# Performance work log

Hardware: AMD Instinct MI355X
Metric: run time of the kernel (lower is better)

## Reference

```python
import jax, jax.numpy as jnp
import numpy as np

K = 3  # kernel size per dim
PAD = K // 2
CHANS = [1, 40, 80, 160, 80, 40, 1]  # channel ladder of the 6 convNd layers


def conv4d(x, w, b):
    """4D convolution, stride 1, 'same' padding.
    x: [B, Cin, D1, D2, D3, D4]; w: [Cout, Cin, K, K, K, K]; b: [Cout].
    Implemented as K shifted 3D convs along D1 (D1 folded into batch), summed.
    """
    B, Cin, D1, D2, D3, D4 = x.shape
    Cout = w.shape[0]
    # pad only D1 here; the inner conv pads D2..D4
    xp = jnp.pad(x, ((0, 0), (0, 0), (PAD, PAD), (0, 0), (0, 0), (0, 0)))
    xp = jnp.transpose(xp, (0, 2, 1, 3, 4, 5))  # [B, D1+2p, Cin, D2, D3, D4]
    dn = jax.lax.conv_dimension_numbers(
        (B * D1, Cin, D2, D3, D4), (Cout, Cin, K, K, K),
        ('NCDHW', 'OIDHW', 'NCDHW'))
    acc = None
    for i in range(K):  # small fixed loop over kernel taps along D1
        xs = xp[:, i:i + D1].reshape(B * D1, Cin, D2, D3, D4)
        y = jax.lax.conv_general_dilated(
            xs, w[:, :, i], window_strides=(1, 1, 1),
            padding=[(PAD, PAD)] * 3, dimension_numbers=dn)
        acc = y if acc is None else acc + y
    out = acc.reshape(B, D1, Cout, D2, D3, D4)
    out = jnp.transpose(out, (0, 2, 1, 3, 4, 5))
    return out + b[None, :, None, None, None, None]


def setup_inputs() -> dict:
    key = jax.random.key(0)
    kx, key = jax.random.split(key)
    inp = {'x': jax.random.normal(kx, (2, 1, 16, 16, 16, 16), dtype=jnp.float32)}
    for l in range(6):
        kw, key = jax.random.split(key)
        cin, cout = CHANS[l], CHANS[l + 1]
        std = (2.0 / (cin * K ** 4)) ** 0.5  # Kaiming-style fan-in init
        inp[f'w{l + 1}'] = jax.random.normal(kw, (cout, cin, K, K, K, K), dtype=jnp.float32) * std
        inp[f'b{l + 1}'] = jnp.zeros((cout,), dtype=jnp.float32)
    return inp


def reference(x, w1, b1, w2, b2, w3, b3, w4, b4, w5, b5, w6, b6):
    h = jax.nn.relu(conv4d(x, w1, b1))
    h = jax.nn.relu(conv4d(h, w2, b2))
    h = jax.nn.relu(conv4d(h, w3, b3))
    h = jax.nn.relu(conv4d(h, w4, b4))
    h = jax.nn.relu(conv4d(h, w5, b5))
    h = conv4d(h, w6, b6)
    return jax.nn.relu(h)
```

## Files before the change

kernel.cpp:

```cpp
#include <hip/hip_runtime.h>

typedef __attribute__((ext_vector_type(8))) short short8;
typedef __attribute__((ext_vector_type(4))) float f32x4;

#define GLD16(gsrc, ldst) __builtin_amdgcn_global_load_lds( \
    (const __attribute__((address_space(1))) unsigned int*)(gsrc), \
    (__attribute__((address_space(3))) unsigned int*)(ldst), 16, 0, 0)

__device__ __forceinline__ ushort f2bf(float f){
    union { float f; unsigned u; } v; v.f = f;
    unsigned r = (v.u + 0x7fffu + ((v.u >> 16) & 1u)) >> 16;
    return (ushort)r;
}
__device__ __forceinline__ float bf2f(ushort u){
    union { unsigned u; float f; } v; v.u = ((unsigned)u) << 16;
    return v.f;
}

__global__ __launch_bounds__(256) void conv_l1(
    const float* __restrict__ x, const float* __restrict__ w,
    const float* __restrict__ bias, ushort* __restrict__ out)
{
    __shared__ float xs[2916];
    __shared__ float wsh[3240];
    const int tid = threadIdx.x;
    const int bx = blockIdx.x;
    const int d2 = bx & 15, d1 = (bx >> 4) & 15, b = bx >> 8;
    const float* xb = x + (size_t)b * 65536;

    for (int i = tid; i < 2916; i += 256){
        int i4 = i % 18; int r1 = i / 18; int i3 = r1 % 18;
        int r2 = r1 / 18; int a2 = r2 % 3; int a1 = r2 / 3;
        int e1 = d1 + a1 - 1, e2 = d2 + a2 - 1, e3 = i3 - 1, e4 = i4 - 1;
        float v = 0.f;
        if ((unsigned)e1 < 16u && (unsigned)e2 < 16u && (unsigned)e3 < 16u && (unsigned)e4 < 16u)
            v = xb[((e1 * 16 + e2) * 16 + e3) * 16 + e4];
        xs[i] = v;
    }
    for (int i = tid; i < 3240; i += 256) wsh[i] = w[i];
    __syncthreads();

    const int d3 = tid >> 4, d4 = tid & 15;
    float acc[40];
    #pragma unroll
    for (int c = 0; c < 40; ++c) acc[c] = 0.f;

    for (int t1 = 0; t1 < 3; ++t1)
    for (int t2 = 0; t2 < 3; ++t2)
    for (int t3 = 0; t3 < 3; ++t3)
    #pragma unroll
    for (int t4 = 0; t4 < 3; ++t4){
        float xv = xs[((t1 * 3 + t2) * 18 + d3 + t3) * 18 + d4 + t4];
        int tap = ((t1 * 3 + t2) * 3 + t3) * 3 + t4;
        #pragma unroll
        for (int c = 0; c < 40; ++c) acc[c] += wsh[c * 81 + tap] * xv;
    }

    ushort* ob = out + ((size_t)bx * 256 + tid) * 64;
    #pragma unroll
    for (int c = 0; c < 40; ++c){
        float v = acc[c] + bias[c]; v = v > 0.f ? v : 0.f;
        ob[c] = f2bf(v);
    }
    #pragma unroll
    for (int c = 40; c < 64; ++c) ob[c] = 0;
}

__global__ __launch_bounds__(256) void conv_l6(
    const ushort* __restrict__ in, const float* __restrict__ w,
    const float* __restrict__ bias, float* __restrict__ out)
{
    __shared__ float wsh[3240];
    const int tid = threadIdx.x;
    const int bx = blockIdx.x;
    const int d2 = bx & 15, d1 = (bx >> 4) & 15, b = bx >> 8;
    for (int i = tid; i < 3240; i += 256) wsh[i] = w[i];
    __syncthreads();

    const int d3 = tid >> 4, d4 = tid & 15;
    const ushort* inb = in + (size_t)b * 65536 * 48;
    float acc = 0.f;
    for (int t1 = 0; t1 < 3; ++t1){
        int e1 = d1 + t1 - 1; if ((unsigned)e1 >= 16u) continue;
        for (int t2 = 0; t2 < 3; ++t2){
            int e2 = d2 + t2 - 1; if ((unsigned)e2 >= 16u) continue;
            for (int t3 = 0; t3 < 3; ++t3){
                int e3 = d3 + t3 - 1; if ((unsigned)e3 >= 16u) continue;
                for (int t4 = 0; t4 < 3; ++t4){
                    int e4 = d4 + t4 - 1; if ((unsigned)e4 >= 16u) continue;
                    const ushort* p = inb + (size_t)(((e1 * 16 + e2) * 16 + e3) * 16 + e4) * 48;
                    int tap = ((t1 * 3 + t2) * 3 + t3) * 3 + t4;
                    #pragma unroll
                    for (int c8 = 0; c8 < 5; ++c8){
                        short8 v = *(const short8*)(p + c8 * 8);
                        #pragma unroll
                        for (int j = 0; j < 8; ++j)
                            acc += bf2f((ushort)v[j]) * wsh[(c8 * 8 + j) * 81 + tap];
                    }
                }
            }
        }
    }
    float v = acc + bias[0]; v = v > 0.f ? v : 0.f;
    out[(size_t)bx * 256 + tid] = v;
}

__global__ void repack_wq(const float* __restrict__ w, ushort* __restrict__ wq,
                          int cin_real, int cout_real, int kc, int cout_w, int nstrip)
{
    const int ncc = 27 * kc;
    const int total = nstrip * ncc * 8192;
    for (int o = blockIdx.x * blockDim.x + threadIdx.x; o < total; o += gridDim.x * blockDim.x){
        const int j = o & 7;
        const int u_phys = (o >> 3) & 1023;
        const int chunk = o >> 13;
        const int strip = chunk / ncc;
        const int cc = chunk - strip * ncc;
        const int gg = cc / (kc * 3);
        const int rem = cc - gg * (kc * 3);
        const int kh = rem / 3;
        const int t3 = rem - kh * 3;
        float v = 0.f;
        if (u_phys < 12 * cout_w){
            const int per = 4 * cout_w;
            const int gk = ((u_phys % per) / cout_w) & 3;
            const int u = u_phys ^ gk;
            const int t4 = u / per;
            const int rest = u - t4 * per;
            const int gk2 = rest / cout_w;
            const int col = rest - gk2 * cout_w;
            const int tap = gg * 9 + t3 * 3 + t4;
            const int ci = kh * 32 + gk2 * 8 + j;
            const int co = strip * cout_w + col;
            if (ci < cin_real && co < cout_real)
                v = w[((size_t)co * cin_real + ci) * 81 + tap];
        }
        wq[o] = f2bf(v);
    }
}

template<int CIN_S, int COUT_W, int OST, int CREAL, int PADC>
__global__ __launch_bounds__(256, 2) void conv16(
    const ushort* __restrict__ in, const ushort* __restrict__ wq,
    const float* __restrict__ bias, ushort* __restrict__ out)
{
    constexpr int KC  = CIN_S / 32;
    constexpr int NT  = COUT_W / 16;
    constexpr int NCC = 27 * KC;
    constexpr int AH  = 18 * 18 * 32;

    __shared__ __attribute__((aligned(16))) ushort As[2][AH];
    __shared__ __attribute__((aligned(16))) ushort Bs[2][8192];

    const int tid  = threadIdx.x;
    const int lane = tid & 63;
    const int wm   = tid >> 6;
    const int r    = lane & 15;
    const int g    = lane >> 4;

    const int p0 = blockIdx.x;
    const int strip = p0 >> 9;
    const int pp = p0 & 511;
    const int bx = (pp & 7) * 64 + (pp >> 3);
    const int d2 = bx & 15, d1 = (bx >> 4) & 15, b = bx >> 8;
    const int co_base = strip * COUT_W;

    const ushort* inb = in + (size_t)b * 65536 * CIN_S;
    const ushort* wqs = wq + ((size_t)strip * NCC << 13);

    unsigned long long gpack = 0ull; int ng = 0;
    #pragma unroll
    for (int gg = 0; gg < 9; ++gg){
        const int t1 = gg / 3, t2 = gg - (gg / 3) * 3;
        if ((unsigned)(d1 + t1 - 1) < 16u && (unsigned)(d2 + t2 - 1) < 16u){
            gpack |= ((unsigned long long)gg) << (ng * 4);
            ++ng;
        }
    }
    const int nchunk = ng * KC;
    const int nstep  = nchunk * 3;

    f32x4 acc[4][NT];
    #pragma unroll
    for (int mi = 0; mi < 4; ++mi)
        #pragma unroll
        for (int n = 0; n < NT; ++n)
            acc[mi][n] = (f32x4){0.f, 0.f, 0.f, 0.f};

    const int ubase = (tid >> 6) * 256;
    const int ul = tid & 63;

    auto issueB = [&](int sn, ushort* dst){
        const int cc = sn / 3, tt = sn - cc * 3;
        const int gi = cc / KC, kh = cc - gi * KC;
        const int gg = (int)((gpack >> (gi * 4)) & 15ull);
        const ushort* src = wqs + ((size_t)((gg * KC + kh) * 3 + tt) << 13);
        #pragma unroll
        for (int k = 0; k < 4; ++k){
            const int u0 = ubase + k * 64;
            GLD16(src + (size_t)(u0 + ul) * 8, dst + u0 * 8);
        }
    };
    auto issueA = [&](int cn, ushort* dst){
        const int gi = cn / KC, kh = cn - gi * KC;
        const int gg = (int)((gpack >> (gi * 4)) & 15ull);
        const int t1 = gg / 3, t2 = gg - t1 * 3;
        const ushort* src = inb + ((size_t)((d1 + t1 - 1) * 16 + (d2 + t2 - 1)) * 256) * CIN_S + kh * 32;
        const int e4s = ul >> 2;
        const int gcs = (ul & 3) ^ ((ul >> 3) & 3);
        #pragma unroll
        for (int k = 0; k < 4; ++k){
            const int row = wm * 4 + k;
            GLD16(src + (size_t)(row * 16 + e4s) * CIN_S + gcs * 8,
                  dst + ((row + 1) * 18 + 1) * 32);
        }
    };

    {
        const short8 z = {0, 0, 0, 0, 0, 0, 0, 0};
        short8* a0 = (short8*)As[0];
        short8* a1 = (short8*)As[1];
        for (int i = tid; i < AH / 8; i += 256){ a0[i] = z; a1[i] = z; }
    }
    asm volatile("s_waitcnt lgkmcnt(0)" ::: "memory");
    __builtin_amdgcn_s_barrier();
    issueA(0, As[0]);
    issueB(0, Bs[0]);
    asm volatile("s_waitcnt vmcnt(0)" ::: "memory");
    __builtin_amdgcn_s_barrier();
    __builtin_amdgcn_sched_barrier(0);

    int c = 0, t3 = 0;
    for (int s = 0; s < nstep; ++s){
        int nis = 0;
        if (s + 1 < nstep){ issueB(s + 1, Bs[(s + 1) & 1]); nis += 4; }
        if (t3 == 0 && c + 1 < nchunk){ issueA(c + 1, As[(c + 1) & 1]); nis += 4; }
        if (nis == 8)      asm volatile("s_waitcnt vmcnt(8)" ::: "memory");
        else if (nis == 4) asm volatile("s_waitcnt vmcnt(4)" ::: "memory");
        else               asm volatile("s_waitcnt vmcnt(0)" ::: "memory");
        __builtin_amdgcn_s_barrier();
        __builtin_amdgcn_sched_barrier(0);

        const ushort* Ab = As[c & 1];
        const ushort* Bb = Bs[s & 1];
        __builtin_amdgcn_s_setprio(1);
        #pragma unroll
        for (int t4 = 0; t4 < 3; ++t4){
            const int e4 = r + t4 - 1;
            const int gsw = (g ^ ((e4 >> 1) & 3)) * 8;
            const ushort* arow = Ab + ((wm * 4 + t3) * 18 + (e4 + 1)) * 32 + gsw;
            short8 bfr[NT];
            #pragma unroll
            for (int n = 0; n < NT; ++n)
                bfr[n] = *(const short8*)(Bb + ((((t4 * 4 + g) * COUT_W + n * 16 + r) * 8) ^ (g << 3)));
            #pragma unroll
            for (int mi = 0; mi < 4; ++mi){
                const short8 af = *(const short8*)(arow + mi * (18 * 32));
                #pragma unroll
                for (int n = 0; n < NT; ++n)
                    acc[mi][n] = __builtin_amdgcn_mfma_f32_16x16x32_bf16(af, bfr[n], acc[mi][n], 0, 0, 0);
            }
        }
        __builtin_amdgcn_s_setprio(0);

        __builtin_amdgcn_sched_barrier(0);
        __builtin_amdgcn_s_barrier();
        __builtin_amdgcn_sched_barrier(0);

        ++t3; if (t3 == 3){ t3 = 0; ++c; }
    }

    float bv[NT];
    #pragma unroll
    for (int n = 0; n < NT; ++n){
        const int co = co_base + n * 16 + r;
        bv[n] = (co < CREAL) ? bias[co] : 0.f;
    }
    ushort* ob = out + (size_t)bx * 256 * OST;
    #pragma unroll
    for (int mi = 0; mi < 4; ++mi){
        #pragma unroll
        for (int n = 0; n < NT; ++n){
            const int co = co_base + n * 16 + r;
            #pragma unroll
            for (int j = 0; j < 4; ++j){
                const int row = 64 * wm + 16 * mi + g * 4 + j;
                float v = acc[mi][n][j] + bv[n];
                v = v > 0.f ? v : 0.f;
                ob[(size_t)row * OST + co] = f2bf(v);
            }
        }
    }
    if (PADC > 0){
        const int row = 64 * wm + lane;
        const short8 z = {0, 0, 0, 0, 0, 0, 0, 0};
        #pragma unroll
        for (int pc = 0; pc < PADC; pc += 8)
            *(short8*)(ob + (size_t)row * OST + CREAL + pc) = z;
    }
}

extern "C" void kernel_launch(void* const* d_in, const int* in_sizes, int n_in,
                              void* d_out, int out_size, void* d_ws, size_t ws_size,
                              hipStream_t stream) {
    const float* x  = (const float*)d_in[0];
    const float* w1 = (const float*)d_in[1];  const float* b1 = (const float*)d_in[2];
    const float* w2 = (const float*)d_in[3];  const float* b2 = (const float*)d_in[4];
    const float* w3 = (const float*)d_in[5];  const float* b3 = (const float*)d_in[6];
    const float* w4 = (const float*)d_in[7];  const float* b4 = (const float*)d_in[8];
    const float* w5 = (const float*)d_in[9];  const float* b5 = (const float*)d_in[10];
    const float* w6 = (const float*)d_in[11]; const float* b6 = (const float*)d_in[12];

    ushort* bufA = (ushort*)d_ws;
    ushort* bufB = bufA + (size_t)131072 * 160;
    ushort* wq2  = bufB + (size_t)131072 * 96;
    ushort* wq3  = wq2 + (size_t)54  * 8192;
    ushort* wq4  = wq3 + (size_t)162 * 8192;
    ushort* wq5  = wq4 + (size_t)135 * 8192;

    repack_wq<<<512, 256, 0, stream>>>(w2, wq2,  40,  80, 2, 80, 1);
    repack_wq<<<512, 256, 0, stream>>>(w3, wq3,  80, 160, 3, 80, 2);
    repack_wq<<<512, 256, 0, stream>>>(w4, wq4, 160,  80, 5, 80, 1);
    repack_wq<<<512, 256, 0, stream>>>(w5, wq5,  80,  40, 3, 48, 1);

    conv_l1<<<512, 256, 0, stream>>>(x, w1, b1, bufA);
    conv16<  64,   80,  96,  80,  16><<< 512, 256, 0, stream>>>(bufA, wq2, b2, bufB);
    conv16<  96,   80, 160, 160,   0><<<1024, 256, 0, stream>>>(bufB, wq3, b3, bufA);
    conv16< 160,   80,  96,  80,  16><<< 512, 256, 0, stream>>>(bufA, wq4, b4, bufB);
    conv16<  96,   48,  48,  40,   0><<< 512, 256, 0, stream>>>(bufB, wq5, b5, bufA);
    conv_l6<<<512, 256, 0, stream>>>(bufA, w6, b6, (float*)d_out);
}
```

Baseline: 814.0 us.

## Read weights directly from global memory and stage activations through registers

Drops the LDS double buffer for weight tiles: MFMA B fragments are now loaded straight from global memory (L1/L2 cached), and the repack no longer applies an XOR swizzle. Activation tiles are prefetched two chunks ahead into registers and written to LDS with ordinary stores, replacing the direct global-to-LDS async loads. Per-step barriers fall to one per chunk, and occupancy is raised to 3 blocks per CU because LDS use drops. In exchange, weight reads now stall the MFMA loop on global latency instead of being hidden behind an async prefetch, and register pressure goes up.

```diff
diff --git a/kernel.cpp b/kernel.cpp
--- a/kernel.cpp
+++ b/kernel.cpp
@@ -2,10 +2,6 @@
 
 typedef __attribute__((ext_vector_type(8))) short short8;
 typedef __attribute__((ext_vector_type(4))) float f32x4;
-
-#define GLD16(gsrc, ldst) __builtin_amdgcn_global_load_lds( \
-    (const __attribute__((address_space(1))) unsigned int*)(gsrc), \
-    (__attribute__((address_space(3))) unsigned int*)(ldst), 16, 0, 0)
 
 __device__ __forceinline__ ushort f2bf(float f){
     union { float f; unsigned u; } v; v.f = f;
@@ -112,7 +108,7 @@
     const int total = nstrip * ncc * 8192;
     for (int o = blockIdx.x * blockDim.x + threadIdx.x; o < total; o += gridDim.x * blockDim.x){
         const int j = o & 7;
-        const int u_phys = (o >> 3) & 1023;
+        const int u = (o >> 3) & 1023;
         const int chunk = o >> 13;
         const int strip = chunk / ncc;
         const int cc = chunk - strip * ncc;
@@ -121,16 +117,14 @@
         const int kh = rem / 3;
         const int t3 = rem - kh * 3;
         float v = 0.f;
-        if (u_phys < 12 * cout_w){
+        if (u < 12 * cout_w){
             const int per = 4 * cout_w;
-            const int gk = ((u_phys % per) / cout_w) & 3;
-            const int u = u_phys ^ gk;
             const int t4 = u / per;
             const int rest = u - t4 * per;
-            const int gk2 = rest / cout_w;
-            const int col = rest - gk2 * cout_w;
+            const int gk = rest / cout_w;
+            const int col = rest - gk * cout_w;
             const int tap = gg * 9 + t3 * 3 + t4;
-            const int ci = kh * 32 + gk2 * 8 + j;
+            const int ci = kh * 32 + gk * 8 + j;
             const int co = strip * cout_w + col;
             if (ci < cin_real && co < cout_real)
                 v = w[((size_t)co * cin_real + ci) * 81 + tap];
@@ -140,7 +134,7 @@
 }
 
 template<int CIN_S, int COUT_W, int OST, int CREAL, int PADC>
-__global__ __launch_bounds__(256, 2) void conv16(
+__global__ __launch_bounds__(256, 3) void conv16(
     const ushort* __restrict__ in, const ushort* __restrict__ wq,
     const float* __restrict__ bias, ushort* __restrict__ out)
 {
@@ -150,7 +144,6 @@
     constexpr int AH  = 18 * 18 * 32;
 
     __shared__ __attribute__((aligned(16))) ushort As[2][AH];
-    __shared__ __attribute__((aligned(16))) ushort Bs[2][8192];
 
     const int tid  = threadIdx.x;
     const int lane = tid & 63;
@@ -178,7 +171,6 @@
         }
     }
     const int nchunk = ng * KC;
-    const int nstep  = nchunk * 3;
 
     f32x4 acc[4][NT];
     #pragma unroll
@@ -187,32 +179,27 @@
         for (int n = 0; n < NT; ++n)
             acc[mi][n] = (f32x4){0.f, 0.f, 0.f, 0.f};
 
-    const int ubase = (tid >> 6) * 256;
-    const int ul = tid & 63;
-
-    auto issueB = [&](int sn, ushort* dst){
-        const int cc = sn / 3, tt = sn - cc * 3;
-        const int gi = cc / KC, kh = cc - gi * KC;
-        const int gg = (int)((gpack >> (gi * 4)) & 15ull);
-        const ushort* src = wqs + ((size_t)((gg * KC + kh) * 3 + tt) << 13);
-        #pragma unroll
-        for (int k = 0; k < 4; ++k){
-            const int u0 = ubase + k * 64;
-            GLD16(src + (size_t)(u0 + ul) * 8, dst + u0 * 8);
-        }
-    };
-    auto issueA = [&](int cn, ushort* dst){
-        const int gi = cn / KC, kh = cn - gi * KC;
+    short8 areg[4];
+    const int e4s = lane >> 2;
+    const int jl  = lane & 3;
+    const int gcs = jl ^ ((lane >> 3) & 3);
+
+    auto loadAreg = [&](int c){
+        const int gi = c / KC, kh = c - gi * KC;
         const int gg = (int)((gpack >> (gi * 4)) & 15ull);
         const int t1 = gg / 3, t2 = gg - t1 * 3;
         const ushort* src = inb + ((size_t)((d1 + t1 - 1) * 16 + (d2 + t2 - 1)) * 256) * CIN_S + kh * 32;
-        const int e4s = ul >> 2;
-        const int gcs = (ul & 3) ^ ((ul >> 3) & 3);
         #pragma unroll
         for (int k = 0; k < 4; ++k){
             const int row = wm * 4 + k;
-            GLD16(src + (size_t)(row * 16 + e4s) * CIN_S + gcs * 8,
-                  dst + ((row + 1) * 18 + 1) * 32);
+            areg[k] = *(const short8*)(src + (size_t)(row * 16 + e4s) * CIN_S + gcs * 8);
+        }
+    };
+    auto writeA = [&](ushort* dst){
+        #pragma unroll
+        for (int k = 0; k < 4; ++k){
+            const int row = wm * 4 + k;
+            *(short8*)(dst + ((row + 1) * 18 + 1 + e4s) * 32 + jl * 8) = areg[k];
         }
     };
 
@@ -224,50 +211,47 @@
     }
     asm volatile("s_waitcnt lgkmcnt(0)" ::: "memory");
     __builtin_amdgcn_s_barrier();
-    issueA(0, As[0]);
-    issueB(0, Bs[0]);
-    asm volatile("s_waitcnt vmcnt(0)" ::: "memory");
+    loadAreg(0);
+    writeA(As[0]);
+    if (nchunk > 1) loadAreg(1);
+    asm volatile("s_waitcnt lgkmcnt(0)" ::: "memory");
     __builtin_amdgcn_s_barrier();
-    __builtin_amdgcn_sched_barrier(0);
-
-    int c = 0, t3 = 0;
-    for (int s = 0; s < nstep; ++s){
-        int nis = 0;
-        if (s + 1 < nstep){ issueB(s + 1, Bs[(s + 1) & 1]); nis += 4; }
-        if (t3 == 0 && c + 1 < nchunk){ issueA(c + 1, As[(c + 1) & 1]); nis += 4; }
-        if (nis == 8)      asm volatile("s_waitcnt vmcnt(8)" ::: "memory");
-        else if (nis == 4) asm volatile("s_waitcnt vmcnt(4)" ::: "memory");
-        else               asm volatile("s_waitcnt vmcnt(0)" ::: "memory");
-        __builtin_amdgcn_s_barrier();
-        __builtin_amdgcn_sched_barrier(0);
-
+
+    for (int c = 0; c < nchunk; ++c){
+        if (c + 1 < nchunk) writeA(As[(c + 1) & 1]);
+
+        const int gi = c / KC, kh = c - gi * KC;
+        const int gg = (int)((gpack >> (gi * 4)) & 15ull);
         const ushort* Ab = As[c & 1];
-        const ushort* Bb = Bs[s & 1];
-        __builtin_amdgcn_s_setprio(1);
-        #pragma unroll
-        for (int t4 = 0; t4 < 3; ++t4){
-            const int e4 = r + t4 - 1;
-            const int gsw = (g ^ ((e4 >> 1) & 3)) * 8;
-            const ushort* arow = Ab + ((wm * 4 + t3) * 18 + (e4 + 1)) * 32 + gsw;
-            short8 bfr[NT];
+        const ushort* Bg0 = wqs + ((size_t)((gg * KC + kh) * 3) << 13);
+
+        #pragma unroll
+        for (int t3 = 0; t3 < 3; ++t3){
+            if (t3 == 1 && c + 2 < nchunk) loadAreg(c + 2);
+            const ushort* Bg = Bg0 + ((size_t)t3 << 13);
+            __builtin_amdgcn_s_setprio(1);
             #pragma unroll
-            for (int n = 0; n < NT; ++n)
-                bfr[n] = *(const short8*)(Bb + ((((t4 * 4 + g) * COUT_W + n * 16 + r) * 8) ^ (g << 3)));
-            #pragma unroll
-            for (int mi = 0; mi < 4; ++mi){
-                const short8 af = *(const short8*)(arow + mi * (18 * 32));
+            for (int t4 = 0; t4 < 3; ++t4){
+                const int e4 = r + t4 - 1;
+                const int gsw = (g ^ ((e4 >> 1) & 3)) * 8;
+                const ushort* arow = Ab + ((wm * 4 + t3) * 18 + (e4 + 1)) * 32 + gsw;
+                short8 bfr[NT];
                 #pragma unroll
                 for (int n = 0; n < NT; ++n)
-                    acc[mi][n] = __builtin_amdgcn_mfma_f32_16x16x32_bf16(af, bfr[n], acc[mi][n], 0, 0, 0);
+                    bfr[n] = *(const short8*)(Bg + ((t4 * 4 + g) * COUT_W + n * 16 + r) * 8);
+                #pragma unroll
+                for (int mi = 0; mi < 4; ++mi){
+                    const short8 af = *(const short8*)(arow + mi * (18 * 32));
+                    #pragma unroll
+                    for (int n = 0; n < NT; ++n)
+                        acc[mi][n] = __builtin_amdgcn_mfma_f32_16x16x32_bf16(af, bfr[n], acc[mi][n], 0, 0, 0);
+                }
             }
-        }
-        __builtin_amdgcn_s_setprio(0);
-
-        __builtin_amdgcn_sched_barrier(0);
+            __builtin_amdgcn_s_setprio(0);
+        }
+
+        asm volatile("s_waitcnt lgkmcnt(0)" ::: "memory");
         __builtin_amdgcn_s_barrier();
-        __builtin_amdgcn_sched_barrier(0);
-
-        ++t3; if (t3 == 3){ t3 = 0; ++c; }
     }
 
     float bv[NT];
```

Result: slower. 885.3 us (+8.8%).
